# Optimization experiments

Measured on AMD Instinct MI355X. Metric: run time of the kernel, lower is better.

## Reference

```python
import jax, jax.numpy as jnp
import numpy as np
from jax import lax

DIM = 128
K = 3
PAD = K // 2


def setup_inputs() -> dict:
    key = jax.random.key(0)
    k1, k2, k3, k4, k5 = jax.random.split(key, 5)
    B, H, W = 64, 32, 32
    wdim = DIM * DIM * K * K + DIM  # 147584
    # scale question_rep (it encodes conv weights) for numerical sanity
    question_rep = jax.random.normal(k1, (B, wdim), dtype=jnp.float32) * 0.05
    lhs_rep = jax.random.normal(k2, (B, DIM, H, W), dtype=jnp.float32)
    rhs_rep = jax.random.normal(k3, (B, DIM, H, W), dtype=jnp.float32)
    proj_w = jax.random.normal(k4, (DIM, 2 * DIM), dtype=jnp.float32) * (1.0 / np.sqrt(2 * DIM))
    proj_b = jax.random.normal(k5, (DIM,), dtype=jnp.float32) * 0.01
    return {"question_rep": question_rep, "lhs_rep": lhs_rep,
            "rhs_rep": rhs_rep, "proj_w": proj_w, "proj_b": proj_b}


def _per_sample_conv(x, w, b):
    # x: [dim, H, W], w: [dim, dim, K, K], b: [dim]
    y = lax.conv_general_dilated(
        x[None], w, window_strides=(1, 1),
        padding=[(PAD, PAD), (PAD, PAD)],
        dimension_numbers=("NCHW", "OIHW", "NCHW"))
    return y[0] + b[:, None, None]


def reference(question_rep, lhs_rep, rhs_rep, proj_w, proj_b):
    B = question_rep.shape[0]
    wdim = DIM * DIM * K * K
    cnn_weight = question_rep[:, :wdim].reshape(B, DIM, DIM, K, K)
    cnn_bias = question_rep[:, wdim:]  # [B, dim]
    # 1x1 projection conv: cat along channels then contract
    cat = jnp.concatenate([lhs_rep, rhs_rep], axis=1)  # [B, 2*dim, H, W]
    cnn_inp = jnp.einsum("bchw,oc->bohw", cat, proj_w) + proj_b[None, :, None, None]
    # per-sample dynamic conv, vectorized over batch (equiv. grouped conv)
    out = jax.vmap(_per_sample_conv)(cnn_inp, cnn_weight, cnn_bias)
    return out
```

## Files before the change

kernel.cpp:

```cpp
#include <hip/hip_runtime.h>
#include <hip/hip_bf16.h>

#define QSTRIDE 147584
#define WOFF    147456

typedef __attribute__((ext_vector_type(8))) short bf16x8;
typedef __attribute__((ext_vector_type(4))) float f32x4;

static __device__ __forceinline__ ushort f2bf(float f) {
  union { float f; unsigned u; } x; x.f = f;
  unsigned r = x.u + 0x7fffu + ((x.u >> 16) & 1u);
  return (ushort)(r >> 16);
}
static __device__ __forceinline__ unsigned pk2(ushort a, ushort b) {
  return (unsigned)a | ((unsigned)b << 16);
}
static __device__ __forceinline__ void async16(const ushort* g, ushort* l) {
  __builtin_amdgcn_global_load_lds((const __attribute__((address_space(1))) void*)g,
                                   (__attribute__((address_space(3))) void*)l, 16, 0, 0);
}

__global__ __launch_bounds__(256) void pack_w_kernel(const float* __restrict__ q,
                                                     ushort* __restrict__ wt2) {
  __shared__ float Ls[4608];
  int b = blockIdx.x >> 3, ogrp = blockIdx.x & 7;
  int t = threadIdx.x;
  const float* gbase = q + (size_t)b * QSTRIDE + (size_t)ogrp * 16 * 1152;
  ushort* dstb = wt2 + (size_t)b * 147456;
  int o_loc = t >> 6;
  int ci    = (t & 63) * 2;
  int cq    = ci >> 5, coff = ci & 31;
  for (int r = 0; r < 4; ++r) {
    __syncthreads();
    const float* gs = gbase + r * 4608;
#pragma unroll
    for (int i = 0; i < 18; ++i) Ls[i * 256 + t] = gs[i * 256 + t];
    __syncthreads();
    int o_full = ogrp * 16 + r * 4 + o_loc;
    const float* v = Ls + o_loc * 1152 + ci * 9;
    float a[18];
#pragma unroll
    for (int i = 0; i < 18; ++i) a[i] = v[i];
    ushort* dd = dstb + (size_t)cq * 4096 + o_full * 32 + coff;
#pragma unroll
    for (int tap = 0; tap < 9; ++tap) {
      unsigned pkv = pk2(f2bf(a[tap]), f2bf(a[9 + tap]));
      *(unsigned*)(dd + (size_t)tap * 16384) = pkv;
    }
  }
}

__global__ __launch_bounds__(256) void pack_pw_kernel(const float* __restrict__ pw,
                                                      ushort* __restrict__ pwb2) {
  int tg = blockIdx.x * 256 + threadIdx.x;
  int o  = tg >> 5;
  int c0 = (tg & 31) * 8;
  const float4* s4 = (const float4*)(pw + (size_t)o * 256 + c0);
  float4 f0 = s4[0], f1 = s4[1];
  uint4 pkv;
  pkv.x = pk2(f2bf(f0.x), f2bf(f0.y)); pkv.y = pk2(f2bf(f0.z), f2bf(f0.w));
  pkv.z = pk2(f2bf(f1.x), f2bf(f1.y)); pkv.w = pk2(f2bf(f1.z), f2bf(f1.w));
  *(uint4*)(pwb2 + (size_t)(c0 >> 5) * 4096 + o * 32 + (c0 & 31)) = pkv;
}

__global__ __launch_bounds__(256) void zero_border_kernel(ushort* __restrict__ xp2) {
  int b = blockIdx.x, t = threadIdx.x;
  for (int idx = t; idx < 528; idx += 256) {
    int cq = idx / 132, r = idx - cq * 132;
    int hp, wp;
    if (r < 34)       { hp = 0;        wp = r; }
    else if (r < 68)  { hp = 33;       wp = r - 34; }
    else if (r < 100) { hp = r - 67;   wp = 0; }
    else              { hp = r - 99;   wp = 33; }
    uint4 z = {0u,0u,0u,0u};
    uint4* dst = (uint4*)(xp2 + (((size_t)b * 4 + cq) * 1156 + hp * 34 + wp) * 32);
#pragma unroll
    for (int i = 0; i < 4; ++i) dst[i] = z;
  }
}

__global__ __launch_bounds__(256, 2) void proj_kernel(const ushort* __restrict__ pwb2,
                                                      const float* __restrict__ lhs,
                                                      const float* __restrict__ rhs,
                                                      const float* __restrict__ pb,
                                                      ushort* __restrict__ xp2) {
  __shared__ ushort As[128 * 32];
  __shared__ ushort Bs[128 * 32];
  int b = blockIdx.y, tile = blockIdx.x;
  int p0 = tile * 128;
  int t = threadIdx.x;
  int lane = t & 63, wv = t >> 6;
  int m0 = (wv & 1) * 64, n0 = (wv >> 1) * 64;
  int quad = lane >> 4, li = lane & 15;
  f32x4 acc[4][4] = {};
  int cgrp = t & 3;
  int pq   = t >> 2;

  for (int c0 = 0; c0 < 256; c0 += 32) {
    const float* src = (c0 < 128 ? lhs : rhs) + (size_t)b * 131072
                     + (size_t)((c0 & 127) + cgrp * 8) * 1024 + p0 + 2 * pq;
    ushort u0[8], u1[8];
#pragma unroll
    for (int j = 0; j < 8; ++j) {
      float2 f = *(const float2*)(src + (size_t)j * 1024);
      u0[j] = f2bf(f.x); u1[j] = f2bf(f.y);
    }
    __syncthreads();
    {
      const ushort* ag = pwb2 + (size_t)(c0 >> 5) * 4096;
      async16(ag + (size_t)wv * 512 + lane * 8,       As + wv * 512);
      async16(ag + (size_t)(wv + 4) * 512 + lane * 8, As + (wv + 4) * 512);
    }
    {
      uint4 pk0, pk1;
      pk0.x = pk2(u0[0],u0[1]); pk0.y = pk2(u0[2],u0[3]);
      pk0.z = pk2(u0[4],u0[5]); pk0.w = pk2(u0[6],u0[7]);
      pk1.x = pk2(u1[0],u1[1]); pk1.y = pk2(u1[2],u1[3]);
      pk1.z = pk2(u1[4],u1[5]); pk1.w = pk2(u1[6],u1[7]);
      *(uint4*)(Bs + (size_t)(2*pq)   * 32 + cgrp * 8) = pk0;
      *(uint4*)(Bs + (size_t)(2*pq+1) * 32 + cgrp * 8) = pk1;
    }
    __syncthreads();
    bf16x8 af[4], bg[4];
#pragma unroll
    for (int mi = 0; mi < 4; ++mi)
      af[mi] = *(const bf16x8*)(As + (m0 + mi*16 + li) * 32 + quad * 8);
#pragma unroll
    for (int ni = 0; ni < 4; ++ni)
      bg[ni] = *(const bf16x8*)(Bs + (n0 + ni*16 + li) * 32 + quad * 8);
#pragma unroll
    for (int mi = 0; mi < 4; ++mi)
#pragma unroll
      for (int ni = 0; ni < 4; ++ni)
        acc[mi][ni] = __builtin_amdgcn_mfma_f32_16x16x32_bf16(af[mi], bg[ni], acc[mi][ni], 0, 0, 0);
  }

  ushort* xpb = xp2 + (size_t)b * 4 * 1156 * 32;
#pragma unroll
  for (int mi = 0; mi < 4; ++mi) {
    int o0 = m0 + mi*16 + quad*4;
    float4 bias = *(const float4*)(pb + o0);
#pragma unroll
    for (int ni = 0; ni < 4; ++ni) {
      int p = p0 + n0 + ni*16 + li;
      int h = p >> 5, w = p & 31;
      ushort* dp = xpb + ((size_t)(o0 >> 5) * 1156 + (h + 1) * 34 + (w + 1)) * 32 + (o0 & 31);
      f32x4 a = acc[mi][ni];
      uint2 pkv;
      pkv.x = pk2(f2bf(a.x + bias.x), f2bf(a.y + bias.y));
      pkv.y = pk2(f2bf(a.z + bias.z), f2bf(a.w + bias.w));
      *(uint2*)dp = pkv;
    }
  }
}

__global__ __launch_bounds__(256, 2) void conv_kernel(const ushort* __restrict__ wt2,
                                                      const ushort* __restrict__ xp2,
                                                      const float* __restrict__ q,
                                                      float* __restrict__ out) {
  __shared__ ushort As[2][4096];
  __shared__ ushort Bs[6528];
  int blk = blockIdx.x;
  int b = blk & 63, tile = blk >> 6;
  int p0 = tile * 128, h0 = tile * 4;
  int t = threadIdx.x;
  int lane = t & 63, wv = t >> 6;
  int m0 = (wv & 1) * 64, n0 = (wv >> 1) * 64;
  int quad = lane >> 4, li = lane & 15;
  f32x4 acc[4][4] = {};
  const ushort* wtb = wt2 + (size_t)b * 147456;
  const ushort* xpb = xp2 + (size_t)b * 147968;

  for (int cq = 0; cq < 4; ++cq) {
    __syncthreads();
    {
      const ushort* bgp = xpb + (size_t)(cq * 1156 + h0 * 34) * 32;
#pragma unroll
      for (int p = 0; p < 3; ++p)
        async16(bgp + (size_t)(p * 256 + t) * 8, Bs + p * 2048 + wv * 512);
      if (t < 48)
        async16(bgp + (size_t)(768 + t) * 8, Bs + 6144);
    }
    {
      const ushort* ag = wtb + (size_t)cq * 4096;
      async16(ag + (size_t)t * 8,         As[0] + wv * 512);
      async16(ag + (size_t)(256 + t) * 8, As[0] + 2048 + wv * 512);
    }
    for (int tap = 0; tap < 9; ++tap) {
      __syncthreads();
      if (tap < 8) {
        const ushort* ag = wtb + (size_t)((tap + 1) * 4 + cq) * 4096;
        ushort* ab = As[(tap + 1) & 1];
        async16(ag + (size_t)t * 8,         ab + wv * 512);
        async16(ag + (size_t)(256 + t) * 8, ab + 2048 + wv * 512);
      }
      int kh = tap / 3, kw = tap - kh * 3;
      const ushort* ar = As[tap & 1];
      bf16x8 af[4], bg[4];
#pragma unroll
      for (int mi = 0; mi < 4; ++mi)
        af[mi] = *(const bf16x8*)(ar + (m0 + mi*16 + li) * 32 + quad * 8);
#pragma unroll
      for (int ni = 0; ni < 4; ++ni) {
        int pl = n0 + ni*16 + li;
        int h = pl >> 5, w = pl & 31;
        bg[ni] = *(const bf16x8*)(Bs + ((h + kh) * 34 + (w + kw)) * 32 + quad * 8);
      }
#pragma unroll
      for (int mi = 0; mi < 4; ++mi)
#pragma unroll
        for (int ni = 0; ni < 4; ++ni)
          acc[mi][ni] = __builtin_amdgcn_mfma_f32_16x16x32_bf16(af[mi], bg[ni], acc[mi][ni], 0, 0, 0);
    }
  }

  const float* qb = q + (size_t)b * QSTRIDE + WOFF;
  float* ob = out + (size_t)b * 128 * 1024 + p0;
#pragma unroll
  for (int mi = 0; mi < 4; ++mi) {
    int o0 = m0 + mi*16 + quad*4;
    float4 bias = *(const float4*)(qb + o0);
#pragma unroll
    for (int ni = 0; ni < 4; ++ni) {
      int pl = n0 + ni*16 + li;
      float* dp = ob + (size_t)o0 * 1024 + pl;
      f32x4 a = acc[mi][ni];
      dp[0]    = a.x + bias.x;
      dp[1024] = a.y + bias.y;
      dp[2048] = a.z + bias.z;
      dp[3072] = a.w + bias.w;
    }
  }
}

extern "C" void kernel_launch(void* const* d_in, const int* in_sizes, int n_in,
                              void* d_out, int out_size, void* d_ws, size_t ws_size,
                              hipStream_t stream) {
  const float* q   = (const float*)d_in[0];
  const float* lhs = (const float*)d_in[1];
  const float* rhs = (const float*)d_in[2];
  const float* pw  = (const float*)d_in[3];
  const float* pb  = (const float*)d_in[4];
  float* out = (float*)d_out;

  char* ws = (char*)d_ws;
  ushort* wt2  = (ushort*)(ws);
  ushort* pwb2 = (ushort*)(ws + 18874368);
  ushort* xp2  = (ushort*)(ws + 18939904);

  pack_w_kernel     <<<512, 256, 0, stream>>>(q, wt2);
  pack_pw_kernel    <<<16,  256, 0, stream>>>(pw, pwb2);
  zero_border_kernel<<<64,  256, 0, stream>>>(xp2);
  proj_kernel       <<<dim3(8, 64), 256, 0, stream>>>(pwb2, lhs, rhs, pb, xp2);
  conv_kernel       <<<512, 256, 0, stream>>>(wt2, xp2, q, out);
}
```

Measured before the change: 182.2 us.

## Software-pipeline proj_kernel with double-buffered weight DMA and register prefetch

The projection GEMM loop now double-buffers the weight tile in LDS and prefetches the next chunk of fp32 activations into registers while the current chunk's MFMAs run. The goal is to hide global-load latency behind compute instead of stalling at the top of each iteration. In exchange it uses more LDS and registers, and the hand-placed waitcnt and barrier ordering needs care to stay correct. Only the projection kernel changes; the conv kernel, which probably dominates the time, is untouched.

```diff
diff --git a/kernel.cpp b/kernel.cpp
--- a/kernel.cpp
+++ b/kernel.cpp
@@ -84,8 +84,8 @@
                                                       const float* __restrict__ rhs,
                                                       const float* __restrict__ pb,
                                                       ushort* __restrict__ xp2) {
-  __shared__ ushort As[128 * 32];
-  __shared__ ushort Bs[128 * 32];
+  __shared__ ushort As[2][4096];
+  __shared__ ushort Bs[4096];
   int b = blockIdx.y, tile = blockIdx.x;
   int p0 = tile * 128;
   int t = threadIdx.x;
@@ -96,35 +96,54 @@
   int cgrp = t & 3;
   int pq   = t >> 2;
 
-  for (int c0 = 0; c0 < 256; c0 += 32) {
-    const float* src = (c0 < 128 ? lhs : rhs) + (size_t)b * 131072
-                     + (size_t)((c0 & 127) + cgrp * 8) * 1024 + p0 + 2 * pq;
-    ushort u0[8], u1[8];
-#pragma unroll
-    for (int j = 0; j < 8; ++j) {
-      float2 f = *(const float2*)(src + (size_t)j * 1024);
-      u0[j] = f2bf(f.x); u1[j] = f2bf(f.y);
-    }
-    __syncthreads();
-    {
-      const ushort* ag = pwb2 + (size_t)(c0 >> 5) * 4096;
-      async16(ag + (size_t)wv * 512 + lane * 8,       As + wv * 512);
-      async16(ag + (size_t)(wv + 4) * 512 + lane * 8, As + (wv + 4) * 512);
-    }
-    {
-      uint4 pk0, pk1;
-      pk0.x = pk2(u0[0],u0[1]); pk0.y = pk2(u0[2],u0[3]);
-      pk0.z = pk2(u0[4],u0[5]); pk0.w = pk2(u0[6],u0[7]);
-      pk1.x = pk2(u1[0],u1[1]); pk1.y = pk2(u1[2],u1[3]);
-      pk1.z = pk2(u1[4],u1[5]); pk1.w = pk2(u1[6],u1[7]);
-      *(uint4*)(Bs + (size_t)(2*pq)   * 32 + cgrp * 8) = pk0;
-      *(uint4*)(Bs + (size_t)(2*pq+1) * 32 + cgrp * 8) = pk1;
-    }
-    __syncthreads();
+  const float* base_l = lhs + (size_t)b * 131072 + (size_t)(cgrp * 8) * 1024 + p0 + 2 * pq;
+  const float* base_r = rhs + (size_t)b * 131072 + (size_t)(cgrp * 8) * 1024 + p0 + 2 * pq;
+
+#define PROJ_DMA(c, buf) do { \
+    const ushort* ag_ = pwb2 + (size_t)(c) * 4096; \
+    async16(ag_ + (size_t)wv * 512 + lane * 8,       As[buf] + wv * 512); \
+    async16(ag_ + (size_t)(wv + 4) * 512 + lane * 8, As[buf] + (wv + 4) * 512); \
+  } while (0)
+
+#define PROJ_LOAD(c, fb) do { \
+    const float* src_ = ((c) < 4 ? base_l : base_r) + (size_t)(((c) & 3) * 32) * 1024; \
+    _Pragma("unroll") \
+    for (int j = 0; j < 8; ++j) fb[j] = *(const float2*)(src_ + (size_t)j * 1024); \
+  } while (0)
+
+#define PROJ_PACK(fb) do { \
+    pk0.x = pk2(f2bf(fb[0].x), f2bf(fb[1].x)); \
+    pk0.y = pk2(f2bf(fb[2].x), f2bf(fb[3].x)); \
+    pk0.z = pk2(f2bf(fb[4].x), f2bf(fb[5].x)); \
+    pk0.w = pk2(f2bf(fb[6].x), f2bf(fb[7].x)); \
+    pk1.x = pk2(f2bf(fb[0].y), f2bf(fb[1].y)); \
+    pk1.y = pk2(f2bf(fb[2].y), f2bf(fb[3].y)); \
+    pk1.z = pk2(f2bf(fb[4].y), f2bf(fb[5].y)); \
+    pk1.w = pk2(f2bf(fb[6].y), f2bf(fb[7].y)); \
+  } while (0)
+
+  float2 fb0[8], fb1[8];
+  PROJ_DMA(0, 0);
+  PROJ_LOAD(0, fb0);
+
+#pragma unroll
+  for (int c = 0; c < 8; ++c) {
+    uint4 pk0, pk1;
+    if (c & 1) PROJ_PACK(fb1); else PROJ_PACK(fb0);
+    asm volatile("s_waitcnt lgkmcnt(0)" ::: "memory");
+    __builtin_amdgcn_s_barrier();
+    *(uint4*)(Bs + (size_t)(2*pq)   * 32 + cgrp * 8) = pk0;
+    *(uint4*)(Bs + (size_t)(2*pq+1) * 32 + cgrp * 8) = pk1;
+    __syncthreads();
+    if (c < 7) {
+      PROJ_DMA(c + 1, (c + 1) & 1);
+      if (c & 1) PROJ_LOAD(c + 1, fb0); else PROJ_LOAD(c + 1, fb1);
+    }
+    const ushort* ar = As[c & 1];
     bf16x8 af[4], bg[4];
 #pragma unroll
     for (int mi = 0; mi < 4; ++mi)
-      af[mi] = *(const bf16x8*)(As + (m0 + mi*16 + li) * 32 + quad * 8);
+      af[mi] = *(const bf16x8*)(ar + (m0 + mi*16 + li) * 32 + quad * 8);
 #pragma unroll
     for (int ni = 0; ni < 4; ++ni)
       bg[ni] = *(const bf16x8*)(Bs + (n0 + ni*16 + li) * 32 + quad * 8);
@@ -152,6 +171,9 @@
       *(uint2*)dp = pkv;
     }
   }
+#undef PROJ_DMA
+#undef PROJ_LOAD
+#undef PROJ_PACK
 }
 
 __global__ __launch_bounds__(256, 2) void conv_kernel(const ushort* __restrict__ wt2,
```

Result: no change. 182.2 us (-0.0%).
